# Optimization experiments

Measured on AMD Instinct MI355X. Metric: run time of the kernel, lower is better.

## Reference

```python
import jax, jax.numpy as jnp
import numpy as np

L, D, DM, H, FF = 2048, 32, 1024, 16, 4096
DH = DM // H  # 64
SCALE = float(np.sqrt(DH))


def layernorm(x, g, b, eps=1e-5):
    mu = jnp.mean(x, axis=-1, keepdims=True)
    var = jnp.mean(jnp.square(x - mu), axis=-1, keepdims=True)
    return (x - mu) * jax.lax.rsqrt(var + eps) * g + b


def setup_inputs() -> dict:
    key = jax.random.key(0)
    ks = jax.random.split(key, 8)
    p = lambda k, shp: jax.random.normal(k, shp, jnp.float32) * 0.02
    return {
        "src": jax.random.normal(ks[0], (L, DM), jnp.float32),
        "target": jax.random.normal(ks[1], (L, D, DM), jnp.float32),
        "attn_mask": jnp.zeros((L, D), jnp.float32),
        "Wq": p(ks[2], (DM, DM)), "bq": jnp.zeros((DM,), jnp.float32),
        "Wk": p(ks[3], (DM, DM)), "bk": jnp.zeros((DM,), jnp.float32),
        "Wv": p(ks[4], (DM, DM)), "bv": jnp.zeros((DM,), jnp.float32),
        "W1": p(ks[5], (DM, FF)), "b1": jnp.zeros((FF,), jnp.float32),
        "W2": p(ks[6], (FF, DM)), "b2": jnp.zeros((DM,), jnp.float32),
        "g1": jnp.ones((DM,), jnp.float32), "beta1": jnp.zeros((DM,), jnp.float32),
        "g2": jnp.ones((DM,), jnp.float32), "beta2": jnp.zeros((DM,), jnp.float32),
    }


def reference(src, target, attn_mask, Wq, bq, Wk, bk, Wv, bv,
              W1, b1, W2, b2, g1, beta1, g2, beta2):
    # projections: src (L, DM), target (L, D, DM)
    q = (src @ Wq + bq).reshape(L, H, DH)            # (L, H, DH)
    k = (target @ Wk + bk).reshape(L, D, H, DH)       # (L, D, H, DH)
    v = (target @ Wv + bv).reshape(L, D, H, DH)
    # per-position attention over the D candidates: scores (H, L, D)
    scores = jnp.einsum('lhd,lkhd->hlk', q, k) / SCALE
    scores = scores + attn_mask[None, :, :]
    probs = jax.nn.softmax(scores, axis=-1)
    ctx = jnp.einsum('hlk,lkhd->lhd', probs, v).reshape(L, DM)
    x = layernorm(src + ctx, g1, beta1)
    ff = jax.nn.gelu(x @ W1 + b1, approximate=False) @ W2 + b2
    return layernorm(x + ff, g2, beta2)
```

## Files before the change

### kernel.cpp

```cpp
#include <hip/hip_runtime.h>
#include <hip/hip_bf16.h>

#define L  2048
#define D  32
#define DM 1024
#define H  16
#define DH 64
#define FF 4096

typedef unsigned short u16;
typedef __attribute__((ext_vector_type(8))) short bf16x8;
typedef __attribute__((ext_vector_type(4))) float f32x4;
typedef __attribute__((ext_vector_type(4))) unsigned int u32x4;
typedef __attribute__((ext_vector_type(8))) unsigned short u16x8;
typedef __attribute__((ext_vector_type(4))) unsigned short u16x4;

static __device__ __forceinline__ float bf2f(u16 u) {
    return __uint_as_float(((unsigned)u) << 16);
}
static __device__ __forceinline__ u16 f2bf(float f) {
    union { __hip_bfloat16 b; u16 u; } cv;
    cv.b = __float2bfloat16(f);
    return cv.u;
}
static __device__ __forceinline__ void gll16(const u16* gsrc, u16* ldst) {
    __builtin_amdgcn_global_load_lds(
        (const __attribute__((address_space(1))) unsigned int*)gsrc,
        (__attribute__((address_space(3))) unsigned int*)ldst, 16, 0, 0);
}

__global__ __launch_bounds__(256) void cvt_bf(const float* __restrict__ in,
                                              u16* __restrict__ out, int n4) {
    int i = blockIdx.x * 256 + threadIdx.x;
    if (i < n4) {
        const float4 v = reinterpret_cast<const float4*>(in)[i];
        u16x4 o = { f2bf(v.x), f2bf(v.y), f2bf(v.z), f2bf(v.w) };
        *reinterpret_cast<u16x4*>(out + (long)i * 4) = o;
    }
}

__global__ void cvt_T(const float* __restrict__ in, u16* __restrict__ out, int R, int C) {
    __shared__ float tile[32][33];
    const int tx = threadIdx.x, ty = threadIdx.y;
    const int bx = blockIdx.x * 32, by = blockIdx.y * 32;
    #pragma unroll
    for (int i = 0; i < 32; i += 8)
        tile[ty + i][tx] = in[(long)(by + ty + i) * C + bx + tx];
    __syncthreads();
    #pragma unroll
    for (int i = 0; i < 32; i += 8)
        out[(long)(bx + ty + i) * R + by + tx] = f2bf(tile[tx][ty + i]);
}

#define LDT 40
template<int EPI>
__global__ __launch_bounds__(256) void gemm_bt(
    const u16* __restrict__ A, int lda, long aBS,
    const u16* __restrict__ Bt, int ldb, long bBS,
    void* __restrict__ Cv, int ldc, long cBS,
    const float* __restrict__ bias, int biasBS, int K)
{
    __shared__ u16 As[64 * LDT];
    __shared__ u16 Bs[64 * LDT];
    const int t = threadIdx.x;
    const int z = blockIdx.z;
    const int mBase = blockIdx.y * 64, nBase = blockIdx.x * 64;
    const u16* Ab = A + (long)z * aBS;
    const u16* Bb = Bt + (long)z * bBS;
    const int lane = t & 63, w = t >> 6;
    const int r = t >> 2, seg = t & 3;
    f32x4 acc[4] = { {0.f,0.f,0.f,0.f}, {0.f,0.f,0.f,0.f}, {0.f,0.f,0.f,0.f}, {0.f,0.f,0.f,0.f} };
    const long aRow = (long)(mBase + r) * lda;
    const long bRow = (long)(nBase + r) * ldb;
    for (int k0 = 0; k0 < K; k0 += 32) {
        __syncthreads();
        *reinterpret_cast<u32x4*>(&As[r * LDT + seg * 8]) =
            *reinterpret_cast<const u32x4*>(&Ab[aRow + k0 + seg * 8]);
        *reinterpret_cast<u32x4*>(&Bs[r * LDT + seg * 8]) =
            *reinterpret_cast<const u32x4*>(&Bb[bRow + k0 + seg * 8]);
        __syncthreads();
        const bf16x8 af = *reinterpret_cast<const bf16x8*>(
            &As[(w * 16 + (lane & 15)) * LDT + (lane >> 4) * 8]);
        #pragma unroll
        for (int j = 0; j < 4; ++j) {
            const bf16x8 bfr = *reinterpret_cast<const bf16x8*>(
                &Bs[(j * 16 + (lane & 15)) * LDT + (lane >> 4) * 8]);
            acc[j] = __builtin_amdgcn_mfma_f32_16x16x32_bf16(af, bfr, acc[j], 0, 0, 0);
        }
    }
    const int rbase = mBase + w * 16 + ((lane >> 4) << 2);
    const int cb = nBase + (lane & 15);
    #pragma unroll
    for (int j = 0; j < 4; ++j) {
        const int col = cb + j * 16;
        const float badd = bias ? bias[(long)z * biasBS + col] : 0.f;
        #pragma unroll
        for (int i = 0; i < 4; ++i) {
            float v = acc[j][i] + badd;
            if (EPI == 2) v = 0.5f * v * (1.f + erff(v * 0.70710678118654752f));
            const long off = (long)z * cBS + (long)(rbase + i) * ldc + col;
            if (EPI == 1) reinterpret_cast<float*>(Cv)[off] = v;
            else          reinterpret_cast<u16*>(Cv)[off]  = f2bf(v);
        }
    }
}

template<int EPI>
__global__ __launch_bounds__(256) void gemm128(
    const u16* __restrict__ A, int lda, long aZ,
    const u16* __restrict__ Bt, int ldb, long bZ,
    void* __restrict__ Cv, int ldc, long cZ,
    const float* __restrict__ bias, int K)
{
    __shared__ u16 As[128 * 64];
    __shared__ u16 Bs[128 * 64];
    const int t = threadIdx.x, lane = t & 63, w = t >> 6;
    const int z = blockIdx.z;
    const int mBase = blockIdx.y * 128, nBase = blockIdx.x * 128;
    const u16* Ab = A + (long)z * aZ;
    const u16* Bb = Bt + (long)z * bZ;
    const int wr = w >> 1, wc = w & 1;
    const int sr = lane >> 3, sg = lane & 7, sswz = sg ^ sr;
    f32x4 acc[4][4];
    #pragma unroll
    for (int mi = 0; mi < 4; ++mi)
        #pragma unroll
        for (int ni = 0; ni < 4; ++ni) acc[mi][ni] = (f32x4){0.f, 0.f, 0.f, 0.f};

    for (int k0 = 0; k0 < K; k0 += 64) {
        #pragma unroll
        for (int i = 0; i < 4; ++i) {
            const int r = w * 32 + i * 8 + sr;
            gll16(&Ab[(long)(mBase + r) * lda + k0 + sswz * 8], &As[r * 64 + sg * 8]);
        }
        #pragma unroll
        for (int i = 0; i < 4; ++i) {
            const int r = w * 32 + i * 8 + sr;
            gll16(&Bb[(long)(nBase + r) * ldb + k0 + sswz * 8], &Bs[r * 64 + sg * 8]);
        }
        __syncthreads();
        #pragma unroll
        for (int ks = 0; ks < 2; ++ks) {
            bf16x8 aF[4], bF[4];
            #pragma unroll
            for (int mi = 0; mi < 4; ++mi) {
                const int rr = wr * 64 + mi * 16 + (lane & 15);
                aF[mi] = *reinterpret_cast<const bf16x8*>(
                    &As[rr * 64 + ((ks * 4 + (lane >> 4)) ^ (rr & 7)) * 8]);
            }
            #pragma unroll
            for (int ni = 0; ni < 4; ++ni) {
                const int rr = wc * 64 + ni * 16 + (lane & 15);
                bF[ni] = *reinterpret_cast<const bf16x8*>(
                    &Bs[rr * 64 + ((ks * 4 + (lane >> 4)) ^ (rr & 7)) * 8]);
            }
            #pragma unroll
            for (int mi = 0; mi < 4; ++mi)
                #pragma unroll
                for (int ni = 0; ni < 4; ++ni)
                    acc[mi][ni] = __builtin_amdgcn_mfma_f32_16x16x32_bf16(
                        aF[mi], bF[ni], acc[mi][ni], 0, 0, 0);
        }
        __syncthreads();
    }
    const int rb = mBase + wr * 64 + ((lane >> 4) << 2);
    const int cb = nBase + wc * 64 + (lane & 15);
    #pragma unroll
    for (int mi = 0; mi < 4; ++mi) {
        #pragma unroll
        for (int ni = 0; ni < 4; ++ni) {
            const int col = cb + ni * 16;
            const float badd = bias ? bias[col] : 0.f;
            #pragma unroll
            for (int i = 0; i < 4; ++i) {
                float v = acc[mi][ni][i] + badd;
                if (EPI == 2) v = 0.5f * v * (1.f + erff(v * 0.70710678118654752f));
                const long off = (long)z * cZ + (long)(rb + mi * 16 + i) * ldc + col;
                if (EPI == 1) reinterpret_cast<float*>(Cv)[off] = v;
                else          reinterpret_cast<u16*>(Cv)[off]  = f2bf(v);
            }
        }
    }
}

#define NL 8
template<bool QKLDS>
__global__ __launch_bounds__(512) void attn_mfma(
    const u16* __restrict__ qk,
    const float* __restrict__ target,
    const float* __restrict__ mask,
    u16* __restrict__ tw)
{
    extern __shared__ u16 smem[];
    u16* tgtS = smem;
    u16* qkS  = smem + D * DM;

    const int t = threadIdx.x, lane = t & 63, w = t >> 6;
    const int g = lane >> 4, hm = lane & 15;
    const int l0 = blockIdx.x * NL;

    float4 pf[16];
    u16x8  qf[4];
    {
        const float* tl = target + (long)l0 * (D * DM);
        #pragma unroll
        for (int it = 0; it < 16; ++it)
            pf[it] = reinterpret_cast<const float4*>(tl)[it * 512 + t];
        if (QKLDS) {
            const u16* ql = qk + (long)l0 * (H * DM);
            #pragma unroll
            for (int it = 0; it < 4; ++it)
                qf[it] = reinterpret_cast<const u16x8*>(ql)[it * 512 + t];
        }
    }

    for (int li = 0; li < NL; ++li) {
        const int l = l0 + li;
        #pragma unroll
        for (int it = 0; it < 16; ++it) {
            const int i = it * 512 + t;
            const int d = i >> 8, mm = (i & 255) * 4, cc = mm ^ ((d & 15) << 3);
            u16x4 o = { f2bf(pf[it].x), f2bf(pf[it].y), f2bf(pf[it].z), f2bf(pf[it].w) };
            *reinterpret_cast<u16x4*>(&tgtS[d * DM + cc]) = o;
        }
        if (QKLDS) {
            #pragma unroll
            for (int it = 0; it < 4; ++it) {
                const int i = it * 512 + t;
                const int h = i >> 7, mm = (i & 127) * 8, cc = mm ^ ((h & 15) << 3);
                *reinterpret_cast<u16x8*>(&qkS[h * DM + cc]) = qf[it];
            }
        }
        const float* mrow = mask + (long)l * D;
        float mk[8];
        #pragma unroll
        for (int r = 0; r < 4; ++r) { mk[r] = mrow[4 * g + r]; mk[4 + r] = mrow[16 + 4 * g + r]; }
        __syncthreads();

        if constexpr (QKLDS) {
            if (li < NL - 1) {
                const float* tn = target + (long)(l + 1) * (D * DM);
                #pragma unroll
                for (int it = 0; it < 16; ++it)
                    pf[it] = reinterpret_cast<const float4*>(tn)[it * 512 + t];
                const u16* qn = qk + (long)(l + 1) * (H * DM);
                #pragma unroll
                for (int it = 0; it < 4; ++it)
                    qf[it] = reinterpret_cast<const u16x8*>(qn)[it * 512 + t];
            }
        }

        f32x4 acc0 = {0.f, 0.f, 0.f, 0.f}, acc1 = {0.f, 0.f, 0.f, 0.f};
        const u16* qrow = qk + (long)l * (H * DM) + hm * DM;
        const int swz = hm << 3;
        #pragma unroll 4
        for (int ks = 0; ks < 32; ++ks) {
            const int mcol = ks * 32 + g * 8;
            bf16x8 yf;
            if (QKLDS) yf = *reinterpret_cast<const bf16x8*>(&qkS[hm * DM + (mcol ^ swz)]);
            else       yf = *reinterpret_cast<const bf16x8*>(&qrow[mcol]);
            const bf16x8 x0 = *reinterpret_cast<const bf16x8*>(&tgtS[hm * DM + (mcol ^ swz)]);
            const bf16x8 x1 = *reinterpret_cast<const bf16x8*>(&tgtS[(16 + hm) * DM + (mcol ^ swz)]);
            acc0 = __builtin_amdgcn_mfma_f32_16x16x32_bf16(x0, yf, acc0, 0, 0, 0);
            acc1 = __builtin_amdgcn_mfma_f32_16x16x32_bf16(x1, yf, acc1, 0, 0, 0);
        }

        if constexpr (!QKLDS) {
            if (li < NL - 1) {
                const float* tn = target + (long)(l + 1) * (D * DM);
                #pragma unroll
                for (int it = 0; it < 16; ++it)
                    pf[it] = reinterpret_cast<const float4*>(tn)[it * 512 + t];
            }
        }

        float sc[8];
        #pragma unroll
        for (int r = 0; r < 4; ++r) {
            sc[r]     = acc0[r] * 0.125f + mk[r];
            sc[4 + r] = acc1[r] * 0.125f + mk[4 + r];
        }
        float mx = sc[0];
        #pragma unroll
        for (int r = 1; r < 8; ++r) mx = fmaxf(mx, sc[r]);
        mx = fmaxf(mx, __shfl_xor(mx, 16));
        mx = fmaxf(mx, __shfl_xor(mx, 32));
        float sum = 0.f;
        #pragma unroll
        for (int r = 0; r < 8; ++r) { sc[r] = __expf(sc[r] - mx); sum += sc[r]; }
        sum += __shfl_xor(sum, 16);
        sum += __shfl_xor(sum, 32);
        const float pinv = 1.0f / sum;
        bf16x8 pfrag;
        #pragma unroll
        for (int r = 0; r < 8; ++r) pfrag[r] = (short)f2bf(sc[r] * pinv);

        u16* twl = tw + (long)l * (H * DM);
        const f32x4 zero = {0.f, 0.f, 0.f, 0.f};
        #pragma unroll
        for (int i = 0; i < 8; ++i) {
            const int mg = w * 8 + i;
            const int m = mg * 16 + hm;
            bf16x8 af;
            #pragma unroll
            for (int j = 0; j < 4; ++j) {
                const int d0 = 4 * g + j;
                const int d1 = 16 + 4 * g + j;
                af[j]     = (short)tgtS[d0 * DM + (m ^ (d0 << 3))];
                af[4 + j] = (short)tgtS[d1 * DM + (m ^ (d0 << 3))];
            }
            const f32x4 c = __builtin_amdgcn_mfma_f32_16x16x32_bf16(af, pfrag, zero, 0, 0, 0);
            u16x4 o = { f2bf(c[0]), f2bf(c[1]), f2bf(c[2]), f2bf(c[3]) };
            *reinterpret_cast<u16x4*>(&twl[hm * DM + mg * 16 + 4 * g]) = o;
        }
        __syncthreads();
    }
}

__global__ __launch_bounds__(256) void ln_fuse(
    const float* __restrict__ a, const float* __restrict__ b,
    const float* __restrict__ c, const float* __restrict__ bvec,
    const float* __restrict__ g, const float* __restrict__ be,
    float* __restrict__ o32, u16* __restrict__ o16)
{
    const int l = blockIdx.x, t = threadIdx.x;
    __shared__ float S[4], SS[4];
    __shared__ float stats[2];
    const float4 va = reinterpret_cast<const float4*>(a + (long)l * DM)[t];
    const float4 vb = reinterpret_cast<const float4*>(b + (long)l * DM)[t];
    float v[4] = { va.x + vb.x, va.y + vb.y, va.z + vb.z, va.w + vb.w };
    if (c) {
        const float4 vc = reinterpret_cast<const float4*>(c + (long)l * DM)[t];
        v[0] += vc.x; v[1] += vc.y; v[2] += vc.z; v[3] += vc.w;
    }
    if (bvec) {
        const float4 vv = reinterpret_cast<const float4*>(bvec)[t];
        v[0] += vv.x; v[1] += vv.y; v[2] += vv.z; v[3] += vv.w;
    }
    float s  = v[0] + v[1] + v[2] + v[3];
    float ss = v[0]*v[0] + v[1]*v[1] + v[2]*v[2] + v[3]*v[3];
    #pragma unroll
    for (int off = 32; off; off >>= 1) { s += __shfl_down(s, off); ss += __shfl_down(ss, off); }
    if ((t & 63) == 0) { S[t >> 6] = s; SS[t >> 6] = ss; }
    __syncthreads();
    if (t == 0) {
        const float St  = S[0] + S[1] + S[2] + S[3];
        const float SSt = SS[0] + SS[1] + SS[2] + SS[3];
        const float mu  = St * (1.f / DM);
        const float var = fmaxf(SSt * (1.f / DM) - mu * mu, 0.f);
        stats[0] = mu;
        stats[1] = rsqrtf(var + 1e-5f);
    }
    __syncthreads();
    const float mu = stats[0], rs = stats[1];
    const int c0 = t * 4;
    float ov[4];
    #pragma unroll
    for (int j = 0; j < 4; ++j) ov[j] = (v[j] - mu) * rs * g[c0 + j] + be[c0 + j];
    float4 o; o.x = ov[0]; o.y = ov[1]; o.z = ov[2]; o.w = ov[3];
    reinterpret_cast<float4*>(o32 + (long)l * DM)[t] = o;
    if (o16) {
        u16x4 q = { f2bf(ov[0]), f2bf(ov[1]), f2bf(ov[2]), f2bf(ov[3]) };
        *reinterpret_cast<u16x4*>(o16 + (long)l * DM + c0) = q;
    }
}

extern "C" void kernel_launch(void* const* d_in, const int* in_sizes, int n_in,
                              void* d_out, int out_size, void* d_ws, size_t ws_size,
                              hipStream_t stream)
{
    const float* src    = (const float*)d_in[0];
    const float* target = (const float*)d_in[1];
    const float* amask  = (const float*)d_in[2];
    const float* Wq = (const float*)d_in[3];
    const float* bq = (const float*)d_in[4];
    const float* Wk = (const float*)d_in[5];
    const float* Wv = (const float*)d_in[7];
    const float* bv = (const float*)d_in[8];
    const float* W1 = (const float*)d_in[9];
    const float* b1 = (const float*)d_in[10];
    const float* W2 = (const float*)d_in[11];
    const float* b2 = (const float*)d_in[12];
    const float* g1  = (const float*)d_in[13];
    const float* be1 = (const float*)d_in[14];
    const float* g2  = (const float*)d_in[15];
    const float* be2 = (const float*)d_in[16];

    char* ws = (char*)d_ws;
    const size_t MB = (size_t)1 << 20;
    u16*   src16 = (u16*)  (ws +  0 * MB);
    u16*   Wk16  = (u16*)  (ws +  4 * MB);
    u16*   WqT   = (u16*)  (ws +  6 * MB);
    u16*   WvT   = (u16*)  (ws +  8 * MB);
    u16*   W1T   = (u16*)  (ws + 10 * MB);
    u16*   W2T   = (u16*)  (ws + 18 * MB);
    u16*   Q16   = (u16*)  (ws + 26 * MB);
    u16*   qk16  = (u16*)  (ws + 30 * MB);
    u16*   Y16   = (u16*)  (ws + 30 * MB);
    float* Z32   = (float*)(ws + 46 * MB);
    float* Z32b  = Z32 + (long)L * DM;
    float* ctx32 = (float*)(ws + 54 * MB);
    float* x32   = (float*)(ws + 62 * MB);
    u16*   x16   = (u16*)  (ws + 70 * MB);
    u16*   tw16  = (u16*)  (ws + 94 * MB);

    cvt_bf<<<2048, 256, 0, stream>>>(src, src16, (L * DM) / 4);
    cvt_bf<<<1024, 256, 0, stream>>>(Wk, Wk16, (DM * DM) / 4);
    dim3 tb(32, 8);
    cvt_T<<<dim3(32, 32),  tb, 0, stream>>>(Wq, WqT, DM, DM);
    cvt_T<<<dim3(32, 32),  tb, 0, stream>>>(Wv, WvT, DM, DM);
    cvt_T<<<dim3(128, 32), tb, 0, stream>>>(W1, W1T, DM, FF);
    cvt_T<<<dim3(32, 128), tb, 0, stream>>>(W2, W2T, FF, DM);

    gemm_bt<0><<<dim3(DM / 64, L / 64, 1), 256, 0, stream>>>(
        src16, DM, 0, WqT, DM, 0, Q16, DM, 0, bq, 0, DM);
    gemm_bt<0><<<dim3(DM / 64, L / 64, H), 256, 0, stream>>>(
        Q16, DM, DH, Wk16, DM, DH, qk16, H * DM, DM, nullptr, 0, DH);

    (void)hipGetLastError();
    (void)hipFuncSetAttribute(reinterpret_cast<const void*>(&attn_mfma<true>),
                              hipFuncAttributeMaxDynamicSharedMemorySize, 96 * 1024);
    attn_mfma<true><<<L / NL, 512, 96 * 1024, stream>>>(qk16, target, amask, tw16);
    if (hipGetLastError() != hipSuccess) {
        attn_mfma<false><<<L / NL, 512, 64 * 1024, stream>>>(qk16, target, amask, tw16);
    }

    gemm_bt<1><<<dim3(1, L / 64, H), 256, 0, stream>>>(
        tw16, H * DM, DM, WvT, DM, (long)DH * DM, ctx32, DM, DH, bv, DH, DM);
    ln_fuse<<<L, 256, 0, stream>>>(src, ctx32, nullptr, nullptr, g1, be1, x32, x16);
    gemm128<2><<<dim3(FF / 128, L / 128, 1), 256, 0, stream>>>(
        x16, DM, 0, W1T, DM, 0, Y16, FF, 0, b1, DM);
    gemm128<1><<<dim3(DM / 128, L / 128, 2), 256, 0, stream>>>(
        Y16, FF, 2048, W2T, FF, 2048, Z32, DM, (long)L * DM, nullptr, 2048);
    ln_fuse<<<L, 256, 0, stream>>>(x32, Z32, Z32b, b2, g2, be2, (float*)d_out, nullptr);
}
```

Measured before the change: 298.6 us.

## Split attention score reduction across warps and use 128-tile GEMMs for Q/QK

```diff
diff --git a/kernel.cpp b/kernel.cpp
--- a/kernel.cpp
+++ b/kernel.cpp
@@ -183,38 +183,125 @@
     }
 }
 
-#define NL 8
-template<bool QKLDS>
-__global__ __launch_bounds__(512) void attn_mfma(
+#define NLV4 4
+__global__ __launch_bounds__(512, 4) void attn_v4(
     const u16* __restrict__ qk,
     const float* __restrict__ target,
     const float* __restrict__ mask,
     u16* __restrict__ tw)
 {
     extern __shared__ u16 smem[];
-    u16* tgtS = smem;
-    u16* qkS  = smem + D * DM;
+    u16*   tgtS = smem;
+    f32x4* red  = (f32x4*)(smem + D * DM);
 
     const int t = threadIdx.x, lane = t & 63, w = t >> 6;
     const int g = lane >> 4, hm = lane & 15;
-    const int l0 = blockIdx.x * NL;
-
+    const int l0 = blockIdx.x * NLV4;
+
+    for (int li = 0; li < NLV4; ++li) {
+        const int l = l0 + li;
+        const float* tl = target + (long)l * (D * DM);
+        #pragma unroll
+        for (int it = 0; it < 16; ++it) {
+            const int i = it * 512 + t;
+            const float4 v = reinterpret_cast<const float4*>(tl)[i];
+            const int d = i >> 8, mm = (i & 255) * 4, cc = mm ^ ((d & 15) << 3);
+            u16x4 o = { f2bf(v.x), f2bf(v.y), f2bf(v.z), f2bf(v.w) };
+            *reinterpret_cast<u16x4*>(&tgtS[d * DM + cc]) = o;
+        }
+        const float* mrow = mask + (long)l * D;
+        float mk[8];
+        #pragma unroll
+        for (int r = 0; r < 4; ++r) { mk[r] = mrow[4 * g + r]; mk[4 + r] = mrow[16 + 4 * g + r]; }
+        const u16* qbase = qk + (long)l * (H * DM) + hm * DM + w * 128 + g * 8;
+        bf16x8 qc[4];
+        #pragma unroll
+        for (int ks = 0; ks < 4; ++ks)
+            qc[ks] = *reinterpret_cast<const bf16x8*>(&qbase[ks * 32]);
+        __syncthreads();
+
+        f32x4 a0 = {0.f, 0.f, 0.f, 0.f}, a1 = {0.f, 0.f, 0.f, 0.f};
+        const int swz = hm << 3;
+        #pragma unroll
+        for (int ks = 0; ks < 4; ++ks) {
+            const int mcol = w * 128 + ks * 32 + g * 8;
+            const bf16x8 x0 = *reinterpret_cast<const bf16x8*>(&tgtS[hm * DM + (mcol ^ swz)]);
+            const bf16x8 x1 = *reinterpret_cast<const bf16x8*>(&tgtS[(16 + hm) * DM + (mcol ^ swz)]);
+            a0 = __builtin_amdgcn_mfma_f32_16x16x32_bf16(x0, qc[ks], a0, 0, 0, 0);
+            a1 = __builtin_amdgcn_mfma_f32_16x16x32_bf16(x1, qc[ks], a1, 0, 0, 0);
+        }
+        red[(w * 2 + 0) * 64 + lane] = a0;
+        red[(w * 2 + 1) * 64 + lane] = a1;
+        __syncthreads();
+
+        f32x4 s0 = red[lane], s1 = red[64 + lane];
+        #pragma unroll
+        for (int ww = 1; ww < 8; ++ww) {
+            s0 += red[(ww * 2 + 0) * 64 + lane];
+            s1 += red[(ww * 2 + 1) * 64 + lane];
+        }
+
+        float sc[8];
+        #pragma unroll
+        for (int r = 0; r < 4; ++r) {
+            sc[r]     = s0[r] * 0.125f + mk[r];
+            sc[4 + r] = s1[r] * 0.125f + mk[4 + r];
+        }
+        float mx = sc[0];
+        #pragma unroll
+        for (int r = 1; r < 8; ++r) mx = fmaxf(mx, sc[r]);
+        mx = fmaxf(mx, __shfl_xor(mx, 16));
+        mx = fmaxf(mx, __shfl_xor(mx, 32));
+        float sum = 0.f;
+        #pragma unroll
+        for (int r = 0; r < 8; ++r) { sc[r] = __expf(sc[r] - mx); sum += sc[r]; }
+        sum += __shfl_xor(sum, 16);
+        sum += __shfl_xor(sum, 32);
+        const float pinv = 1.0f / sum;
+        bf16x8 pfrag;
+        #pragma unroll
+        for (int r = 0; r < 8; ++r) pfrag[r] = (short)f2bf(sc[r] * pinv);
+
+        u16* twl = tw + (long)l * (H * DM);
+        const f32x4 zero = {0.f, 0.f, 0.f, 0.f};
+        #pragma unroll
+        for (int i = 0; i < 8; ++i) {
+            const int mg = w * 8 + i;
+            const int m = mg * 16 + hm;
+            bf16x8 af;
+            #pragma unroll
+            for (int j = 0; j < 4; ++j) {
+                const int d0 = 4 * g + j;
+                const int d1 = 16 + 4 * g + j;
+                af[j]     = (short)tgtS[d0 * DM + (m ^ (d0 << 3))];
+                af[4 + j] = (short)tgtS[d1 * DM + (m ^ (d0 << 3))];
+            }
+            const f32x4 c = __builtin_amdgcn_mfma_f32_16x16x32_bf16(af, pfrag, zero, 0, 0, 0);
+            u16x4 o = { f2bf(c[0]), f2bf(c[1]), f2bf(c[2]), f2bf(c[3]) };
+            *reinterpret_cast<u16x4*>(&twl[hm * DM + mg * 16 + 4 * g]) = o;
+        }
+        __syncthreads();
+    }
+}
+
+#define NLFB 8
+__global__ __launch_bounds__(512) void attn_fb(
+    const u16* __restrict__ qk, const float* __restrict__ target,
+    const float* __restrict__ mask, u16* __restrict__ tw)
+{
+    extern __shared__ u16 smem[];
+    u16* tgtS = smem;
+    const int t = threadIdx.x, lane = t & 63, w = t >> 6;
+    const int g = lane >> 4, hm = lane & 15;
+    const int l0 = blockIdx.x * NLFB;
     float4 pf[16];
-    u16x8  qf[4];
     {
         const float* tl = target + (long)l0 * (D * DM);
         #pragma unroll
         for (int it = 0; it < 16; ++it)
             pf[it] = reinterpret_cast<const float4*>(tl)[it * 512 + t];
-        if (QKLDS) {
-            const u16* ql = qk + (long)l0 * (H * DM);
-            #pragma unroll
-            for (int it = 0; it < 4; ++it)
-                qf[it] = reinterpret_cast<const u16x8*>(ql)[it * 512 + t];
-        }
-    }
-
-    for (int li = 0; li < NL; ++li) {
+    }
+    for (int li = 0; li < NLFB; ++li) {
         const int l = l0 + li;
         #pragma unroll
         for (int it = 0; it < 16; ++it) {
@@ -223,57 +310,29 @@
             u16x4 o = { f2bf(pf[it].x), f2bf(pf[it].y), f2bf(pf[it].z), f2bf(pf[it].w) };
             *reinterpret_cast<u16x4*>(&tgtS[d * DM + cc]) = o;
         }
-        if (QKLDS) {
-            #pragma unroll
-            for (int it = 0; it < 4; ++it) {
-                const int i = it * 512 + t;
-                const int h = i >> 7, mm = (i & 127) * 8, cc = mm ^ ((h & 15) << 3);
-                *reinterpret_cast<u16x8*>(&qkS[h * DM + cc]) = qf[it];
-            }
-        }
         const float* mrow = mask + (long)l * D;
         float mk[8];
         #pragma unroll
         for (int r = 0; r < 4; ++r) { mk[r] = mrow[4 * g + r]; mk[4 + r] = mrow[16 + 4 * g + r]; }
         __syncthreads();
-
-        if constexpr (QKLDS) {
-            if (li < NL - 1) {
-                const float* tn = target + (long)(l + 1) * (D * DM);
-                #pragma unroll
-                for (int it = 0; it < 16; ++it)
-                    pf[it] = reinterpret_cast<const float4*>(tn)[it * 512 + t];
-                const u16* qn = qk + (long)(l + 1) * (H * DM);
-                #pragma unroll
-                for (int it = 0; it < 4; ++it)
-                    qf[it] = reinterpret_cast<const u16x8*>(qn)[it * 512 + t];
-            }
-        }
-
         f32x4 acc0 = {0.f, 0.f, 0.f, 0.f}, acc1 = {0.f, 0.f, 0.f, 0.f};
         const u16* qrow = qk + (long)l * (H * DM) + hm * DM;
         const int swz = hm << 3;
         #pragma unroll 4
         for (int ks = 0; ks < 32; ++ks) {
             const int mcol = ks * 32 + g * 8;
-            bf16x8 yf;
-            if (QKLDS) yf = *reinterpret_cast<const bf16x8*>(&qkS[hm * DM + (mcol ^ swz)]);
-            else       yf = *reinterpret_cast<const bf16x8*>(&qrow[mcol]);
+            const bf16x8 yf = *reinterpret_cast<const bf16x8*>(&qrow[mcol]);
             const bf16x8 x0 = *reinterpret_cast<const bf16x8*>(&tgtS[hm * DM + (mcol ^ swz)]);
             const bf16x8 x1 = *reinterpret_cast<const bf16x8*>(&tgtS[(16 + hm) * DM + (mcol ^ swz)]);
             acc0 = __builtin_amdgcn_mfma_f32_16x16x32_bf16(x0, yf, acc0, 0, 0, 0);
             acc1 = __builtin_amdgcn_mfma_f32_16x16x32_bf16(x1, yf, acc1, 0, 0, 0);
         }
-
-        if constexpr (!QKLDS) {
-            if (li < NL - 1) {
-                const float* tn = target + (long)(l + 1) * (D * DM);
-                #pragma unroll
-                for (int it = 0; it < 16; ++it)
-                    pf[it] = reinterpret_cast<const float4*>(tn)[it * 512 + t];
-            }
-        }
-
+        if (li < NLFB - 1) {
+            const float* tn = target + (long)(l + 1) * (D * DM);
+            #pragma unroll
+            for (int it = 0; it < 16; ++it)
+                pf[it] = reinterpret_cast<const float4*>(tn)[it * 512 + t];
+        }
         float sc[8];
         #pragma unroll
         for (int r = 0; r < 4; ++r) {
@@ -294,7 +353,6 @@
         bf16x8 pfrag;
         #pragma unroll
         for (int r = 0; r < 8; ++r) pfrag[r] = (short)f2bf(sc[r] * pinv);
-
         u16* twl = tw + (long)l * (H * DM);
         const f32x4 zero = {0.f, 0.f, 0.f, 0.f};
         #pragma unroll
@@ -412,17 +470,17 @@
     cvt_T<<<dim3(128, 32), tb, 0, stream>>>(W1, W1T, DM, FF);
     cvt_T<<<dim3(32, 128), tb, 0, stream>>>(W2, W2T, FF, DM);
 
-    gemm_bt<0><<<dim3(DM / 64, L / 64, 1), 256, 0, stream>>>(
-        src16, DM, 0, WqT, DM, 0, Q16, DM, 0, bq, 0, DM);
-    gemm_bt<0><<<dim3(DM / 64, L / 64, H), 256, 0, stream>>>(
-        Q16, DM, DH, Wk16, DM, DH, qk16, H * DM, DM, nullptr, 0, DH);
+    gemm128<0><<<dim3(DM / 128, L / 128, 1), 256, 0, stream>>>(
+        src16, DM, 0, WqT, DM, 0, Q16, DM, 0, bq, DM);
+    gemm128<0><<<dim3(DM / 128, L / 128, H), 256, 0, stream>>>(
+        Q16, DM, DH, Wk16, DM, DH, qk16, H * DM, DM, nullptr, DH);
 
     (void)hipGetLastError();
-    (void)hipFuncSetAttribute(reinterpret_cast<const void*>(&attn_mfma<true>),
-                              hipFuncAttributeMaxDynamicSharedMemorySize, 96 * 1024);
-    attn_mfma<true><<<L / NL, 512, 96 * 1024, stream>>>(qk16, target, amask, tw16);
+    (void)hipFuncSetAttribute(reinterpret_cast<const void*>(&attn_v4),
+                              hipFuncAttributeMaxDynamicSharedMemorySize, 80 * 1024);
+    attn_v4<<<L / NLV4, 512, 80 * 1024, stream>>>(qk16, target, amask, tw16);
     if (hipGetLastError() != hipSuccess) {
-        attn_mfma<false><<<L / NL, 512, 64 * 1024, stream>>>(qk16, target, amask, tw16);
+        attn_fb<<<L / NLFB, 512, 64 * 1024, stream>>>(qk16, target, amask, tw16);
     }
 
     gemm_bt<1><<<dim3(1, L / 64, H), 256, 0, stream>>>(
```

After: 303.9 us. No clear change (+1.8%).
